# Kernel tuning notes

Measured on AMD Instinct MI355X. Metric: run time of the kernel, lower is better.

## Reference

```python
import jax, jax.numpy as jnp
import numpy as np

DELTA = 0.2
TOPK = 10
RECALL_KS = (1, 5, 10)


def setup_inputs() -> dict:
    key = jax.random.key(0)
    k1, k2 = jax.random.split(key)
    B, D = 8192, 256
    x = jax.random.normal(k1, (B, D), dtype=jnp.float32)
    y = jax.random.normal(k2, (B, D), dtype=jnp.float32)
    return {"x": x, "y": y}


def reference(x, y):
    B = x.shape[0]
    # L2-normalize rows (matches x / sqrt(sum(x*x), keepdim))
    xn = x / jnp.sqrt(jnp.sum(x * x, axis=1, keepdims=True))
    yn = y / jnp.sqrt(jnp.sum(y * y, axis=1, keepdims=True))
    sim = xn @ yn.T                      # [B, B]
    diag = jnp.diagonal(sim)             # [B]
    cor = diag[:, None]                  # cor_similarity[i, j] = sim[i, i]
    loss_mat = jnp.maximum(0.0, sim - cor + DELTA) + jnp.maximum(0.0, sim.T - cor + DELTA)
    # zero the diagonal (vectorized version of the python loop)
    loss_mat = loss_mat * (1.0 - jnp.eye(B, dtype=loss_mat.dtype))
    loss = jnp.sum(loss_mat) / B

    # metrics (no grad in original)
    score = sim - cor                    # [B, B]
    _, pred = jax.lax.top_k(score, TOPK)  # [B, 10] indices, descending
    # torch code: pred.t() [10,B] eq arange(B); equivalent untransposed:
    correct = pred == jnp.arange(B)[:, None]          # [B, 10]
    correct_per_rank = jnp.sum(correct, axis=0)        # [10] hits at rank j
    recall = jnp.stack([jnp.sum(correct[:, :k]) for k in RECALL_KS]).astype(jnp.int32)
    # ndcg weight ln(2)/ln(2+j) for rank j (0-based), matching math.log(2)/math.log(2+j)
    w = jnp.log(2.0) / jnp.log(2.0 + jnp.arange(TOPK, dtype=jnp.float32))
    ndcg = jnp.stack([jnp.sum(correct_per_rank[:k].astype(jnp.float32) * w[:k]) for k in RECALL_KS])
    return loss, recall, ndcg
```

## Files before the change

kernel.cpp:

```cpp
#include <hip/hip_runtime.h>
#include <math.h>

#define NB 8192
#define ND 256
#define DELTA_F 0.2f

typedef __attribute__((ext_vector_type(8))) __bf16 bf16x8;
typedef __attribute__((ext_vector_type(4))) __bf16 bf16x4;
typedef __attribute__((ext_vector_type(4))) float f32x4;

__device__ __forceinline__ void gload16(const void* g, void* l) {
  __builtin_amdgcn_global_load_lds(
      (const __attribute__((address_space(1))) void*)g,
      (__attribute__((address_space(3))) void*)l, 16, 0, 0);
}

__global__ __launch_bounds__(256) void normalize_split_k(
    const float* __restrict__ x, const float* __restrict__ y,
    __bf16* __restrict__ Xh, __bf16* __restrict__ Xl,
    __bf16* __restrict__ Yh, __bf16* __restrict__ Yl,
    float* __restrict__ dd, float* __restrict__ loss_accum, int* __restrict__ cnt) {
  const int w = threadIdx.x >> 6, lane = threadIdx.x & 63;
  const int i = blockIdx.x * 4 + w;
  const size_t rbase = (size_t)i * ND;
  const float4 xv = *(const float4*)&x[rbase + lane * 4];
  const float4 yv = *(const float4*)&y[rbase + lane * 4];
  float sxx = xv.x * xv.x + xv.y * xv.y + xv.z * xv.z + xv.w * xv.w;
  float syy = yv.x * yv.x + yv.y * yv.y + yv.z * yv.z + yv.w * yv.w;
  float sxy = xv.x * yv.x + xv.y * yv.y + xv.z * yv.z + xv.w * yv.w;
#pragma unroll
  for (int o = 1; o < 64; o <<= 1) {
    sxx += __shfl_xor(sxx, o, 64);
    syy += __shfl_xor(syy, o, 64);
    sxy += __shfl_xor(sxy, o, 64);
  }
  const float ix = 1.0f / sqrtf(sxx);
  const float iy = 1.0f / sqrtf(syy);
  if (lane == 0) {
    dd[i] = sxy * ix * iy;
    cnt[i] = 0;
    if (i == 0) loss_accum[0] = 0.0f;
  }
  const float xs[4] = {xv.x * ix, xv.y * ix, xv.z * ix, xv.w * ix};
  const float ys[4] = {yv.x * iy, yv.y * iy, yv.z * iy, yv.w * iy};
  bf16x4 xh, xl, yh, yl;
#pragma unroll
  for (int e = 0; e < 4; ++e) {
    const __bf16 h = (__bf16)xs[e];
    xh[e] = h; xl[e] = (__bf16)(xs[e] - (float)h);
    const __bf16 g = (__bf16)ys[e];
    yh[e] = g; yl[e] = (__bf16)(ys[e] - (float)g);
  }
  *(bf16x4*)&Xh[rbase + lane * 4] = xh;
  *(bf16x4*)&Xl[rbase + lane * 4] = xl;
  *(bf16x4*)&Yh[rbase + lane * 4] = yh;
  *(bf16x4*)&Yl[rbase + lane * 4] = yl;
}

__global__ __launch_bounds__(512, 2) void gemm_mfma(
    const __bf16* __restrict__ Xh, const __bf16* __restrict__ Xl,
    const __bf16* __restrict__ Yh, const __bf16* __restrict__ Yl,
    const float* __restrict__ dd,
    float* __restrict__ loss_accum, int* __restrict__ cnt) {
  __shared__ __bf16 sAB[2][4][256][32];
  __shared__ int c_loc[256];
  __shared__ float lred[8];

  const int tid = threadIdx.x;
  const int bid = blockIdx.x;
  const int xcd = bid & 7, idx = bid >> 3;
  const int bi = xcd * 4 + (idx & 3);
  const int bj = (idx >> 5) * 8 + ((idx >> 2) & 7);
  const int row0 = bi * 256, col0 = bj * 256;

  const int lane = tid & 63, wid = tid >> 6;
  const int wr = wid >> 2, wc = wid & 3;
  const int lr = lane & 15, lkc = lane >> 4;

  if (tid < 256) c_loc[tid] = 0;

  const int rowl = tid >> 2;
  const int swz = (tid & 3) ^ ((tid >> 3) & 3);
  const char* const pAh = (const char*)Xh + (size_t)(row0 + rowl) * 512 + swz * 16;
  const char* const pAl = (const char*)Xl + (size_t)(row0 + rowl) * 512 + swz * 16;
  const char* const pBh = (const char*)Yh + (size_t)(col0 + rowl) * 512 + swz * 16;
  const char* const pBl = (const char*)Yl + (size_t)(col0 + rowl) * 512 + swz * 16;
  char* const lds0 = (char*)&sAB[0][0][0][0];

  f32x4 acc[8][4];
#pragma unroll
  for (int m = 0; m < 8; ++m)
#pragma unroll
    for (int n = 0; n < 4; ++n) acc[m][n] = (f32x4)(0.0f);

  auto stage = [&](int t) {
    char* lb = lds0 + (t & 1) * 65536;
    const int ko = t * 64;
    gload16(pAh + ko,         lb + tid * 16);
    gload16(pAh + ko + 65536, lb +  8192 + tid * 16);
    gload16(pAl + ko,         lb + 16384 + tid * 16);
    gload16(pAl + ko + 65536, lb + 24576 + tid * 16);
    gload16(pBh + ko,         lb + 32768 + tid * 16);
    gload16(pBh + ko + 65536, lb + 40960 + tid * 16);
    gload16(pBl + ko,         lb + 49152 + tid * 16);
    gload16(pBl + ko + 65536, lb + 57344 + tid * 16);
  };

  const int cko = (lkc ^ ((lr >> 1) & 3)) * 8;

  stage(0);
#pragma unroll
  for (int t = 0; t < 8; ++t) {
    if (t < 7) stage(t + 1);
    if (t < 7) asm volatile("s_waitcnt vmcnt(8)\n\ts_barrier" ::: "memory");
    else       asm volatile("s_waitcnt vmcnt(0)\n\ts_barrier" ::: "memory");

    const int b = t & 1;
    bf16x8 bh4[4], bl4[4];
#pragma unroll
    for (int n = 0; n < 4; ++n) {
      bh4[n] = *(const bf16x8*)&sAB[b][2][wc * 64 + n * 16 + lr][cko];
      bl4[n] = *(const bf16x8*)&sAB[b][3][wc * 64 + n * 16 + lr][cko];
    }
#pragma unroll
    for (int half = 0; half < 2; ++half) {
      bf16x8 ah4[4], al4[4];
#pragma unroll
      for (int m = 0; m < 4; ++m) {
        const int r = wr * 128 + (half * 4 + m) * 16 + lr;
        ah4[m] = *(const bf16x8*)&sAB[b][0][r][cko];
        al4[m] = *(const bf16x8*)&sAB[b][1][r][cko];
      }
      __builtin_amdgcn_s_setprio(1);
#pragma unroll
      for (int m = 0; m < 4; ++m)
#pragma unroll
        for (int n = 0; n < 4; ++n) {
          f32x4 a = acc[half * 4 + m][n];
          a = __builtin_amdgcn_mfma_f32_16x16x32_bf16(ah4[m], bh4[n], a, 0, 0, 0);
          a = __builtin_amdgcn_mfma_f32_16x16x32_bf16(ah4[m], bl4[n], a, 0, 0, 0);
          a = __builtin_amdgcn_mfma_f32_16x16x32_bf16(al4[m], bh4[n], a, 0, 0, 0);
          acc[half * 4 + m][n] = a;
        }
      __builtin_amdgcn_s_setprio(0);
    }
  }

  float djv[4];
#pragma unroll
  for (int n = 0; n < 4; ++n) djv[n] = dd[col0 + wc * 64 + n * 16 + lr];

  float lsum = 0.f;
#pragma unroll
  for (int m = 0; m < 8; ++m) {
    const int rbase = wr * 128 + m * 16 + lkc * 4;
#pragma unroll
    for (int q = 0; q < 4; ++q) {
      const int gi = row0 + rbase + q;
      const float dival = dd[gi];
      int cl = 0;
#pragma unroll
      for (int n = 0; n < 4; ++n) {
        const int gj = col0 + wc * 64 + n * 16 + lr;
        const float s = acc[m][n][q];
        if (gi != gj) {
          lsum += fmaxf(0.f, s - dival + DELTA_F) + fmaxf(0.f, s - djv[n] + DELTA_F);
          cl += (s > dival) ? 1 : 0;
        }
      }
      cl += __shfl_xor(cl, 1, 64);
      cl += __shfl_xor(cl, 2, 64);
      cl += __shfl_xor(cl, 4, 64);
      cl += __shfl_xor(cl, 8, 64);
      if (lr == 0) atomicAdd(&c_loc[rbase + q], cl);
    }
  }

#pragma unroll
  for (int o = 32; o > 0; o >>= 1) lsum += __shfl_down(lsum, o, 64);
  if (lane == 0) lred[wid] = lsum;
  __syncthreads();
  if (tid == 0) {
    float s = 0.f;
#pragma unroll
    for (int w = 0; w < 8; ++w) s += lred[w];
    atomicAdd(loss_accum, s);
  }
  if (tid < 256) atomicAdd(&cnt[row0 + tid], c_loc[tid]);
}

__global__ __launch_bounds__(256) void finalize_k(
    const float* __restrict__ loss_accum, const int* __restrict__ cnt,
    float* __restrict__ out) {
  const int t = threadIdx.x;
  float a6[6] = {0.f, 0.f, 0.f, 0.f, 0.f, 0.f};
  for (int i = t; i < NB; i += 256) {
    const int c = cnt[i];
    if (c < 10) {
      const float w = 0.69314718055994531f / logf(2.0f + (float)c);
      a6[2] += 1.f; a6[5] += w;
      if (c < 5) { a6[1] += 1.f; a6[4] += w; }
      if (c < 1) { a6[0] += 1.f; a6[3] += w; }
    }
  }
  __shared__ float red[6][4];
#pragma unroll
  for (int j = 0; j < 6; ++j) {
    float v = a6[j];
#pragma unroll
    for (int o = 32; o > 0; o >>= 1) v += __shfl_down(v, o, 64);
    if ((t & 63) == 0) red[j][t >> 6] = v;
  }
  __syncthreads();
  if (t == 0) {
    out[0] = loss_accum[0] / (float)NB;
#pragma unroll
    for (int j = 0; j < 6; ++j)
      out[1 + j] = red[j][0] + red[j][1] + red[j][2] + red[j][3];
  }
}

extern "C" void kernel_launch(void* const* d_in, const int* in_sizes, int n_in,
                              void* d_out, int out_size, void* d_ws, size_t ws_size,
                              hipStream_t stream) {
  const float* x = (const float*)d_in[0];
  const float* y = (const float*)d_in[1];
  float* out = (float*)d_out;

  char* ws = (char*)d_ws;
  float* loss_accum = (float*)ws;
  int* cnt = (int*)(ws + 256);
  float* dd = (float*)(ws + 256 + 32768);

  const size_t splitOff = 256 + 2 * 32768;
  const size_t matB = (size_t)NB * ND * 2;
  __bf16* Xh = (__bf16*)(ws + splitOff);
  __bf16* Xl = (__bf16*)(ws + splitOff + matB);
  __bf16* Yh = (__bf16*)(ws + splitOff + 2 * matB);
  __bf16* Yl = (__bf16*)(ws + splitOff + 3 * matB);

  hipLaunchKernelGGL(normalize_split_k, dim3(NB / 4), dim3(256), 0, stream,
                     x, y, Xh, Xl, Yh, Yl, dd, loss_accum, cnt);
  hipLaunchKernelGGL(gemm_mfma, dim3(1024), dim3(512), 0, stream,
                     Xh, Xl, Yh, Yl, dd, loss_accum, cnt);
  hipLaunchKernelGGL(finalize_k, dim3(1), dim3(256), 0, stream, loss_accum, cnt, out);
}
```

Measured before the change: 139.7 us.

## Interleave MFMA chains across accumulators and add ping-pong barriers per sub-tile

Splits the per-stage A fragment loop into four quarters of two row tiles. Each quarter issues the three split-precision MFMA passes as separate sweeps over eight accumulators, so dependent MFMAs on the same accumulator are no longer back-to-back. It also adds s_barrier around each compute quarter to make wavefronts alternate between LDS loads and MFMA bursts. The extra barriers add synchronisation cost and may stall waves if the phases do not overlap well.

```diff
diff --git a/kernel.cpp b/kernel.cpp
--- a/kernel.cpp
+++ b/kernel.cpp
@@ -123,26 +123,36 @@
       bl4[n] = *(const bf16x8*)&sAB[b][3][wc * 64 + n * 16 + lr][cko];
     }
 #pragma unroll
-    for (int half = 0; half < 2; ++half) {
-      bf16x8 ah4[4], al4[4];
-#pragma unroll
-      for (int m = 0; m < 4; ++m) {
-        const int r = wr * 128 + (half * 4 + m) * 16 + lr;
-        ah4[m] = *(const bf16x8*)&sAB[b][0][r][cko];
-        al4[m] = *(const bf16x8*)&sAB[b][1][r][cko];
+    for (int q = 0; q < 4; ++q) {
+      bf16x8 ah2[2], al2[2];
+#pragma unroll
+      for (int j = 0; j < 2; ++j) {
+        const int r = wr * 128 + (q * 2 + j) * 16 + lr;
+        ah2[j] = *(const bf16x8*)&sAB[b][0][r][cko];
+        al2[j] = *(const bf16x8*)&sAB[b][1][r][cko];
       }
+      asm volatile("s_barrier" ::: "memory");
       __builtin_amdgcn_s_setprio(1);
 #pragma unroll
-      for (int m = 0; m < 4; ++m)
-#pragma unroll
-        for (int n = 0; n < 4; ++n) {
-          f32x4 a = acc[half * 4 + m][n];
-          a = __builtin_amdgcn_mfma_f32_16x16x32_bf16(ah4[m], bh4[n], a, 0, 0, 0);
-          a = __builtin_amdgcn_mfma_f32_16x16x32_bf16(ah4[m], bl4[n], a, 0, 0, 0);
-          a = __builtin_amdgcn_mfma_f32_16x16x32_bf16(al4[m], bh4[n], a, 0, 0, 0);
-          acc[half * 4 + m][n] = a;
-        }
+      for (int j = 0; j < 2; ++j)
+#pragma unroll
+        for (int n = 0; n < 4; ++n)
+          acc[q * 2 + j][n] = __builtin_amdgcn_mfma_f32_16x16x32_bf16(
+              ah2[j], bh4[n], acc[q * 2 + j][n], 0, 0, 0);
+#pragma unroll
+      for (int j = 0; j < 2; ++j)
+#pragma unroll
+        for (int n = 0; n < 4; ++n)
+          acc[q * 2 + j][n] = __builtin_amdgcn_mfma_f32_16x16x32_bf16(
+              ah2[j], bl4[n], acc[q * 2 + j][n], 0, 0, 0);
+#pragma unroll
+      for (int j = 0; j < 2; ++j)
+#pragma unroll
+        for (int n = 0; n < 4; ++n)
+          acc[q * 2 + j][n] = __builtin_amdgcn_mfma_f32_16x16x32_bf16(
+              al2[j], bh4[n], acc[q * 2 + j][n], 0, 0, 0);
       __builtin_amdgcn_s_setprio(0);
+      asm volatile("s_barrier" ::: "memory");
     }
   }
 
```

Measured after the change: 145.4 us. +4.1%, slower.

## Switch split-bf16 GEMM from 16x16x32 to 32x32x16 MFMA tiles

Applied to the files above, without the earlier changes.

Replaces the 16x16x32 bf16 MFMA tiling with 32x32x16 instructions, with 4x2 32x32 accumulator tiles per wave. LDS fragment loads and swizzle indexing are reworked for the new operand layout, and the epilogue is remapped to the 32x32 output layout with an extra shuffle step in the row-count reduction. The aim is fewer LDS reads per FLOP and higher MFMA throughput per instruction. It also adds a second barrier per k-step, which costs synchronization, and 16-wide accumulators may raise register pressure.

```diff
diff --git a/kernel.cpp b/kernel.cpp
--- a/kernel.cpp
+++ b/kernel.cpp
@@ -7,7 +7,7 @@
 
 typedef __attribute__((ext_vector_type(8))) __bf16 bf16x8;
 typedef __attribute__((ext_vector_type(4))) __bf16 bf16x4;
-typedef __attribute__((ext_vector_type(4))) float f32x4;
+typedef __attribute__((ext_vector_type(16))) float f32x16;
 
 __device__ __forceinline__ void gload16(const void* g, void* l) {
   __builtin_amdgcn_global_load_lds(
@@ -75,7 +75,7 @@
 
   const int lane = tid & 63, wid = tid >> 6;
   const int wr = wid >> 2, wc = wid & 3;
-  const int lr = lane & 15, lkc = lane >> 4;
+  const int l31 = lane & 31, hi = lane >> 5;
 
   if (tid < 256) c_loc[tid] = 0;
 
@@ -87,11 +87,11 @@
   const char* const pBl = (const char*)Yl + (size_t)(col0 + rowl) * 512 + swz * 16;
   char* const lds0 = (char*)&sAB[0][0][0][0];
 
-  f32x4 acc[8][4];
-#pragma unroll
-  for (int m = 0; m < 8; ++m)
-#pragma unroll
-    for (int n = 0; n < 4; ++n) acc[m][n] = (f32x4)(0.0f);
+  f32x16 acc[4][2];
+#pragma unroll
+  for (int m = 0; m < 4; ++m)
+#pragma unroll
+    for (int n = 0; n < 2; ++n) acc[m][n] = (f32x16)(0.0f);
 
   auto stage = [&](int t) {
     char* lb = lds0 + (t & 1) * 65536;
@@ -106,7 +106,7 @@
     gload16(pBl + ko + 65536, lb + 57344 + tid * 16);
   };
 
-  const int cko = (lkc ^ ((lr >> 1) & 3)) * 8;
+  const int fsw = (l31 >> 1) & 3;
 
   stage(0);
 #pragma unroll
@@ -116,52 +116,61 @@
     else       asm volatile("s_waitcnt vmcnt(0)\n\ts_barrier" ::: "memory");
 
     const int b = t & 1;
-    bf16x8 bh4[4], bl4[4];
-#pragma unroll
-    for (int n = 0; n < 4; ++n) {
-      bh4[n] = *(const bf16x8*)&sAB[b][2][wc * 64 + n * 16 + lr][cko];
-      bl4[n] = *(const bf16x8*)&sAB[b][3][wc * 64 + n * 16 + lr][cko];
-    }
-#pragma unroll
-    for (int half = 0; half < 2; ++half) {
-      bf16x8 ah4[4], al4[4];
-#pragma unroll
-      for (int m = 0; m < 4; ++m) {
-        const int r = wr * 128 + (half * 4 + m) * 16 + lr;
-        ah4[m] = *(const bf16x8*)&sAB[b][0][r][cko];
-        al4[m] = *(const bf16x8*)&sAB[b][1][r][cko];
-      }
-      __builtin_amdgcn_s_setprio(1);
-#pragma unroll
-      for (int m = 0; m < 4; ++m)
-#pragma unroll
-        for (int n = 0; n < 4; ++n) {
-          f32x4 a = acc[half * 4 + m][n];
-          a = __builtin_amdgcn_mfma_f32_16x16x32_bf16(ah4[m], bh4[n], a, 0, 0, 0);
-          a = __builtin_amdgcn_mfma_f32_16x16x32_bf16(ah4[m], bl4[n], a, 0, 0, 0);
-          a = __builtin_amdgcn_mfma_f32_16x16x32_bf16(al4[m], bh4[n], a, 0, 0, 0);
-          acc[half * 4 + m][n] = a;
-        }
-      __builtin_amdgcn_s_setprio(0);
-    }
-  }
-
-  float djv[4];
-#pragma unroll
-  for (int n = 0; n < 4; ++n) djv[n] = dd[col0 + wc * 64 + n * 16 + lr];
+    bf16x8 bh[2][2], bl[2][2];
+#pragma unroll
+    for (int n = 0; n < 2; ++n) {
+      const int brow = wc * 64 + n * 32 + l31;
+#pragma unroll
+      for (int s = 0; s < 2; ++s) {
+        const int pos = ((s * 2 + hi) ^ fsw) * 8;
+        bh[n][s] = *(const bf16x8*)&sAB[b][2][brow][pos];
+        bl[n][s] = *(const bf16x8*)&sAB[b][3][brow][pos];
+      }
+    }
+    __builtin_amdgcn_s_setprio(1);
+#pragma unroll
+    for (int m = 0; m < 4; ++m) {
+      const int arow = wr * 128 + m * 32 + l31;
+      bf16x8 ah[2], al[2];
+#pragma unroll
+      for (int s = 0; s < 2; ++s) {
+        const int pos = ((s * 2 + hi) ^ fsw) * 8;
+        ah[s] = *(const bf16x8*)&sAB[b][0][arow][pos];
+        al[s] = *(const bf16x8*)&sAB[b][1][arow][pos];
+      }
+#pragma unroll
+      for (int s = 0; s < 2; ++s) {
+#pragma unroll
+        for (int n = 0; n < 2; ++n)
+          acc[m][n] = __builtin_amdgcn_mfma_f32_32x32x16_bf16(ah[s], bh[n][s], acc[m][n], 0, 0, 0);
+#pragma unroll
+        for (int n = 0; n < 2; ++n)
+          acc[m][n] = __builtin_amdgcn_mfma_f32_32x32x16_bf16(ah[s], bl[n][s], acc[m][n], 0, 0, 0);
+#pragma unroll
+        for (int n = 0; n < 2; ++n)
+          acc[m][n] = __builtin_amdgcn_mfma_f32_32x32x16_bf16(al[s], bh[n][s], acc[m][n], 0, 0, 0);
+      }
+    }
+    __builtin_amdgcn_s_setprio(0);
+    asm volatile("s_barrier" ::: "memory");
+  }
+
+  float djv[2];
+#pragma unroll
+  for (int n = 0; n < 2; ++n) djv[n] = dd[col0 + wc * 64 + n * 32 + l31];
 
   float lsum = 0.f;
 #pragma unroll
-  for (int m = 0; m < 8; ++m) {
-    const int rbase = wr * 128 + m * 16 + lkc * 4;
-#pragma unroll
-    for (int q = 0; q < 4; ++q) {
-      const int gi = row0 + rbase + q;
+  for (int m = 0; m < 4; ++m) {
+#pragma unroll
+    for (int q = 0; q < 16; ++q) {
+      const int rloc = wr * 128 + m * 32 + (q & 3) + 8 * (q >> 2) + 4 * hi;
+      const int gi = row0 + rloc;
       const float dival = dd[gi];
       int cl = 0;
 #pragma unroll
-      for (int n = 0; n < 4; ++n) {
-        const int gj = col0 + wc * 64 + n * 16 + lr;
+      for (int n = 0; n < 2; ++n) {
+        const int gj = col0 + wc * 64 + n * 32 + l31;
         const float s = acc[m][n][q];
         if (gi != gj) {
           lsum += fmaxf(0.f, s - dival + DELTA_F) + fmaxf(0.f, s - djv[n] + DELTA_F);
@@ -172,7 +181,8 @@
       cl += __shfl_xor(cl, 2, 64);
       cl += __shfl_xor(cl, 4, 64);
       cl += __shfl_xor(cl, 8, 64);
-      if (lr == 0) atomicAdd(&c_loc[rbase + q], cl);
+      cl += __shfl_xor(cl, 16, 64);
+      if (l31 == 0) atomicAdd(&c_loc[rloc], cl);
     }
   }
 
```

New measurement: 180.1 us. 1.29x slower.

## Interleave tile prefetch with MFMA and fuse finalize into GEMM last block

Applied to the files above, without the earlier changes.

The next k-tile's global-to-LDS loads are now issued in four pieces spread through the compute loop. This lets the loads overlap the LDS reads and MFMA work instead of being issued all at once, at the cost of an extra barrier per iteration. The separate finalize kernel is removed. The last GEMM block to finish, found through an atomic done counter, computes the recall and ndcg reductions, which saves one kernel launch. The trailing reduction is serialized on one block and depends on fences for correctness.

```diff
diff --git a/kernel.cpp b/kernel.cpp
--- a/kernel.cpp
+++ b/kernel.cpp
@@ -19,7 +19,8 @@
     const float* __restrict__ x, const float* __restrict__ y,
     __bf16* __restrict__ Xh, __bf16* __restrict__ Xl,
     __bf16* __restrict__ Yh, __bf16* __restrict__ Yl,
-    float* __restrict__ dd, float* __restrict__ loss_accum, int* __restrict__ cnt) {
+    float* __restrict__ dd, float* __restrict__ loss_accum,
+    int* __restrict__ cnt, int* __restrict__ done_ctr) {
   const int w = threadIdx.x >> 6, lane = threadIdx.x & 63;
   const int i = blockIdx.x * 4 + w;
   const size_t rbase = (size_t)i * ND;
@@ -39,7 +40,7 @@
   if (lane == 0) {
     dd[i] = sxy * ix * iy;
     cnt[i] = 0;
-    if (i == 0) loss_accum[0] = 0.0f;
+    if (i == 0) { loss_accum[0] = 0.0f; *done_ctr = 0; }
   }
   const float xs[4] = {xv.x * ix, xv.y * ix, xv.z * ix, xv.w * ix};
   const float ys[4] = {yv.x * iy, yv.y * iy, yv.z * iy, yv.w * iy};
@@ -61,10 +62,13 @@
     const __bf16* __restrict__ Xh, const __bf16* __restrict__ Xl,
     const __bf16* __restrict__ Yh, const __bf16* __restrict__ Yl,
     const float* __restrict__ dd,
-    float* __restrict__ loss_accum, int* __restrict__ cnt) {
+    float* __restrict__ loss_accum, int* __restrict__ cnt,
+    int* __restrict__ done_ctr, float* __restrict__ out) {
   __shared__ __bf16 sAB[2][4][256][32];
   __shared__ int c_loc[256];
   __shared__ float lred[8];
+  __shared__ float fred[6][8];
+  __shared__ int is_last;
 
   const int tid = threadIdx.x;
   const int bid = blockIdx.x;
@@ -93,26 +97,23 @@
 #pragma unroll
     for (int n = 0; n < 4; ++n) acc[m][n] = (f32x4)(0.0f);
 
-  auto stage = [&](int t) {
-    char* lb = lds0 + (t & 1) * 65536;
+  auto stage_pair = [&](int t, int p) {
+    char* lb = lds0 + (t & 1) * 65536 + p * 16384;
+    const char* src = (p == 0) ? pAh : (p == 1) ? pAl : (p == 2) ? pBh : pBl;
     const int ko = t * 64;
-    gload16(pAh + ko,         lb + tid * 16);
-    gload16(pAh + ko + 65536, lb +  8192 + tid * 16);
-    gload16(pAl + ko,         lb + 16384 + tid * 16);
-    gload16(pAl + ko + 65536, lb + 24576 + tid * 16);
-    gload16(pBh + ko,         lb + 32768 + tid * 16);
-    gload16(pBh + ko + 65536, lb + 40960 + tid * 16);
-    gload16(pBl + ko,         lb + 49152 + tid * 16);
-    gload16(pBl + ko + 65536, lb + 57344 + tid * 16);
+    gload16(src + ko,         lb + tid * 16);
+    gload16(src + ko + 65536, lb + 8192 + tid * 16);
   };
 
   const int cko = (lkc ^ ((lr >> 1) & 3)) * 8;
 
-  stage(0);
+#pragma unroll
+  for (int p = 0; p < 4; ++p) stage_pair(0, p);
+
 #pragma unroll
   for (int t = 0; t < 8; ++t) {
-    if (t < 7) stage(t + 1);
-    if (t < 7) asm volatile("s_waitcnt vmcnt(8)\n\ts_barrier" ::: "memory");
+    if (t < 7) stage_pair(t + 1, 0);
+    if (t < 7) asm volatile("s_waitcnt vmcnt(2)\n\ts_barrier" ::: "memory");
     else       asm volatile("s_waitcnt vmcnt(0)\n\ts_barrier" ::: "memory");
 
     const int b = t & 1;
@@ -122,6 +123,7 @@
       bh4[n] = *(const bf16x8*)&sAB[b][2][wc * 64 + n * 16 + lr][cko];
       bl4[n] = *(const bf16x8*)&sAB[b][3][wc * 64 + n * 16 + lr][cko];
     }
+    if (t < 7) stage_pair(t + 1, 1);
 #pragma unroll
     for (int half = 0; half < 2; ++half) {
       bf16x8 ah4[4], al4[4];
@@ -131,6 +133,7 @@
         ah4[m] = *(const bf16x8*)&sAB[b][0][r][cko];
         al4[m] = *(const bf16x8*)&sAB[b][1][r][cko];
       }
+      if (t < 7) stage_pair(t + 1, 2 + half);
       __builtin_amdgcn_s_setprio(1);
 #pragma unroll
       for (int m = 0; m < 4; ++m)
@@ -144,6 +147,7 @@
         }
       __builtin_amdgcn_s_setprio(0);
     }
+    asm volatile("s_barrier" ::: "memory");
   }
 
   float djv[4];
@@ -187,36 +191,43 @@
     atomicAdd(loss_accum, s);
   }
   if (tid < 256) atomicAdd(&cnt[row0 + tid], c_loc[tid]);
-}
-
-__global__ __launch_bounds__(256) void finalize_k(
-    const float* __restrict__ loss_accum, const int* __restrict__ cnt,
-    float* __restrict__ out) {
-  const int t = threadIdx.x;
-  float a6[6] = {0.f, 0.f, 0.f, 0.f, 0.f, 0.f};
-  for (int i = t; i < NB; i += 256) {
-    const int c = cnt[i];
-    if (c < 10) {
-      const float w = 0.69314718055994531f / logf(2.0f + (float)c);
-      a6[2] += 1.f; a6[5] += w;
-      if (c < 5) { a6[1] += 1.f; a6[4] += w; }
-      if (c < 1) { a6[0] += 1.f; a6[3] += w; }
-    }
-  }
-  __shared__ float red[6][4];
-#pragma unroll
-  for (int j = 0; j < 6; ++j) {
-    float v = a6[j];
-#pragma unroll
-    for (int o = 32; o > 0; o >>= 1) v += __shfl_down(v, o, 64);
-    if ((t & 63) == 0) red[j][t >> 6] = v;
-  }
+
+  __threadfence();
   __syncthreads();
-  if (t == 0) {
-    out[0] = loss_accum[0] / (float)NB;
-#pragma unroll
-    for (int j = 0; j < 6; ++j)
-      out[1 + j] = red[j][0] + red[j][1] + red[j][2] + red[j][3];
+  if (tid == 0) is_last = (atomicAdd(done_ctr, 1) == 1023) ? 1 : 0;
+  __syncthreads();
+  if (is_last) {
+    float a6[6] = {0.f, 0.f, 0.f, 0.f, 0.f, 0.f};
+    for (int i = tid; i < NB; i += 512) {
+      const int c = __hip_atomic_load(&cnt[i], __ATOMIC_RELAXED,
+                                      __HIP_MEMORY_SCOPE_AGENT);
+      if (c < 10) {
+        const float w = 0.69314718055994531f / logf(2.0f + (float)c);
+        a6[2] += 1.f; a6[5] += w;
+        if (c < 5) { a6[1] += 1.f; a6[4] += w; }
+        if (c < 1) { a6[0] += 1.f; a6[3] += w; }
+      }
+    }
+#pragma unroll
+    for (int j = 0; j < 6; ++j) {
+      float v = a6[j];
+#pragma unroll
+      for (int o = 32; o > 0; o >>= 1) v += __shfl_down(v, o, 64);
+      if (lane == 0) fred[j][wid] = v;
+    }
+    __syncthreads();
+    if (tid == 0) {
+      const float lt = __hip_atomic_load(loss_accum, __ATOMIC_RELAXED,
+                                         __HIP_MEMORY_SCOPE_AGENT);
+      out[0] = lt / (float)NB;
+#pragma unroll
+      for (int j = 0; j < 6; ++j) {
+        float s = 0.f;
+#pragma unroll
+        for (int w = 0; w < 8; ++w) s += fred[j][w];
+        out[1 + j] = s;
+      }
+    }
   }
 }
 
@@ -229,6 +240,7 @@
 
   char* ws = (char*)d_ws;
   float* loss_accum = (float*)ws;
+  int* done_ctr = (int*)(ws + 8);
   int* cnt = (int*)(ws + 256);
   float* dd = (float*)(ws + 256 + 32768);
 
@@ -240,8 +252,7 @@
   __bf16* Yl = (__bf16*)(ws + splitOff + 3 * matB);
 
   hipLaunchKernelGGL(normalize_split_k, dim3(NB / 4), dim3(256), 0, stream,
-                     x, y, Xh, Xl, Yh, Yl, dd, loss_accum, cnt);
+                     x, y, Xh, Xl, Yh, Yl, dd, loss_accum, cnt, done_ctr);
   hipLaunchKernelGGL(gemm_mfma, dim3(1024), dim3(512), 0, stream,
-                     Xh, Xl, Yh, Yl, dd, loss_accum, cnt);
-  hipLaunchKernelGGL(finalize_k, dim3(1), dim3(256), 0, stream, loss_accum, cnt, out);
-}
+                     Xh, Xl, Yh, Yl, dd, loss_accum, cnt, done_ctr, out);
+}
```

After: 243.7 us. 74.4% more time.
